# Performance work log

Measured on AMD Instinct MI355X. Metric: run time of the kernel, lower is better.

The kernel has to match this reference:

```python
import jax, jax.numpy as jnp
import numpy as np

EPS = 0.001  # ReEig clamp threshold (init epsilon)


def _eig_fn(x, fn):
    """Batched eigen-decomposition, apply fn to eigenvalues, reconstruct SPD."""
    w, v = jnp.linalg.eigh(x)              # w: [N,d], v: [N,d,d]
    return jnp.einsum('nik,nk,njk->nij', v, fn(w), v)


def reeig(x, eps=EPS):
    return _eig_fn(x, lambda w: jnp.maximum(w, eps))


def logeig(x):
    return _eig_fn(x, jnp.log)


def bimap(x, W):
    # W: [no, ni] (semi-orthogonal), out = W X W^T, SPD of size no
    return jnp.einsum('oi,nij,pj->nop', W, x, W)


def vech(x):
    # Half-vectorization of symmetric matrix; off-diagonal scaled by sqrt(2)
    d = x.shape[-1]
    iu = jnp.triu_indices(d)
    scale = jnp.where(iu[0] == iu[1], 1.0, jnp.sqrt(2.0)).astype(x.dtype)
    return x[:, iu[0], iu[1]] * scale


def _semi_orth(key, no, ni):
    a = jax.random.normal(key, (ni, ni), dtype=jnp.float32)
    q, _ = jnp.linalg.qr(a)
    return q[:no, :]  # [no, ni], rows orthonormal


def setup_inputs() -> dict:
    key = jax.random.key(0)
    kx, k1, k2, k3, kf, kb = jax.random.split(key, 6)
    N, D = 8192, 128
    A = jax.random.normal(kx, (N, D, D), dtype=jnp.float32)
    x = jnp.einsum('nij,nkj->nik', A, A) / D + 1e-3 * jnp.eye(D, dtype=jnp.float32)
    W1 = _semi_orth(k1, 64, 128)
    W2 = _semi_orth(k2, 32, 64)
    W3 = _semi_orth(k3, 16, 32)
    fdim = 16 * 17 // 2  # 136
    fc_w = jax.random.normal(kf, (4, fdim), dtype=jnp.float32) / jnp.sqrt(float(fdim))
    fc_b = jnp.zeros((4,), dtype=jnp.float32)
    return {"x": x, "W1": W1, "W2": W2, "W3": W3, "fc_w": fc_w, "fc_b": fc_b}


def reference(x, W1, W2, W3, fc_w, fc_b):
    h = reeig(bimap(x, W1))
    h = reeig(bimap(h, W2))
    h = reeig(bimap(h, W3))
    h = logeig(h)
    v = vech(h)                       # [N, 136] (dropout is identity in eval)
    return v @ fc_w.T + fc_b          # [N, 4]
```

## Files before the change

### kernel.cpp

```cpp
#include <hip/hip_runtime.h>
#include <math.h>
#include <stdint.h>


typedef __attribute__((ext_vector_type(4))) float f32x4;
typedef __attribute__((ext_vector_type(8))) short bf16x8;
typedef __attribute__((ext_vector_type(4))) unsigned int u32x4;

__constant__ float DCF[21] = {
    -0.98268864f,  1.26902401f, -0.40260548f,  0.17030534f, -0.08104560f,
     0.04113953f, -0.02175295f,  0.01183073f, -0.00656840f,  0.00370465f,
    -0.00211558f,  0.00122033f, -0.00070979f,  0.00041573f, -0.00024495f,
     0.00014506f, -0.00008629f,  0.00005153f, -0.00003088f,  0.00001856f,
    -0.00001119f};

struct Spl { unsigned int h01, h23, l01, l23; };

__device__ __forceinline__ unsigned cvtpk(float a, float b) {
  unsigned r;
  asm("v_cvt_pk_bf16_f32 %0, %1, %2" : "=v"(r) : "v"(a), "v"(b));
  return r;
}

__device__ __forceinline__ Spl split4(const float x[4]) {
  Spl s;
  s.h01 = cvtpk(x[0], x[1]);
  s.h23 = cvtpk(x[2], x[3]);
  const float h0 = __builtin_bit_cast(float, s.h01 << 16);
  const float h1 = __builtin_bit_cast(float, s.h01 & 0xffff0000u);
  const float h2 = __builtin_bit_cast(float, s.h23 << 16);
  const float h3 = __builtin_bit_cast(float, s.h23 & 0xffff0000u);
  s.l01 = cvtpk(x[0] - h0, x[1] - h1);
  s.l23 = cvtpk(x[2] - h2, x[3] - h3);
  return s;
}

__device__ __forceinline__ f32x4 mfma2(u32x4 ua, u32x4 ub, f32x4 acc) {
  return __builtin_amdgcn_mfma_f32_16x16x32_bf16(
      __builtin_bit_cast(bf16x8, ua), __builtin_bit_cast(bf16x8, ub), acc,
      0, 0, 0);
}

__device__ __forceinline__ f32x4 mmA(u32x4 ua, const Spl& b, f32x4 acc) {
  u32x4 ub1 = {b.h01, b.h23, b.h01, b.h23};
  u32x4 ub2 = {b.l01, b.l23, 0u, 0u};
  acc = mfma2(ua, ub1, acc);
  acc = mfma2(ua, ub2, acc);
  return acc;
}

__device__ __forceinline__ f32x4 mmAp(u32x4 ua, u32x4 bp, f32x4 acc) {
  u32x4 ub1 = {bp.x, bp.y, bp.x, bp.y};
  u32x4 ub2 = {bp.z, bp.w, 0u, 0u};
  acc = mfma2(ua, ub1, acc);
  acc = mfma2(ua, ub2, acc);
  return acc;
}

__device__ __forceinline__ f32x4 mmS(const Spl& a, const Spl& b) {
  u32x4 ua = {a.h01, a.h23, a.l01, a.l23};
  f32x4 z = {0.f, 0.f, 0.f, 0.f};
  return mmA(ua, b, z);
}

__global__ __launch_bounds__(256) void ka_weff(const float* __restrict__ W1,
                                               const float* __restrict__ W2,
                                               const float* __restrict__ W3,
                                               u32x4* __restrict__ WDg) {
  __shared__ float W21s[32 * 128];
  __shared__ float Ws[16 * 128];
  const int t = threadIdx.x;
  const int c = t & 127, rb = t >> 7;
  float acc[16];
#pragma unroll
  for (int rr = 0; rr < 16; ++rr) acc[rr] = 0.0f;
  for (int k = 0; k < 64; ++k) {
    const float w1 = W1[k * 128 + c];
#pragma unroll
    for (int rr = 0; rr < 16; ++rr)
      acc[rr] = fmaf(W2[(rb * 16 + rr) * 64 + k], w1, acc[rr]);
  }
#pragma unroll
  for (int rr = 0; rr < 16; ++rr) W21s[(rb * 16 + rr) * 128 + c] = acc[rr];
  __syncthreads();
  float a2[8];
#pragma unroll
  for (int rr = 0; rr < 8; ++rr) a2[rr] = 0.0f;
  for (int k = 0; k < 32; ++k) {
    const float w21 = W21s[k * 128 + c];
#pragma unroll
    for (int rr = 0; rr < 8; ++rr)
      a2[rr] = fmaf(W3[(rb * 8 + rr) * 32 + k], w21, a2[rr]);
  }
#pragma unroll
  for (int rr = 0; rr < 8; ++rr) Ws[(rb * 8 + rr) * 128 + c] = a2[rr];
  __syncthreads();
  {
    const int lane = t & 63, b0 = t >> 6;
    const int g = lane >> 4, cc = lane & 15;
#pragma unroll
    for (int p = 0; p < 2; ++p) {
      const int b = b0 + 4 * p;
      float x[4];
#pragma unroll
      for (int j = 0; j < 4; ++j) x[j] = Ws[cc * 128 + 16 * b + 4 * g + j];
      Spl s = split4(x);
      u32x4 v = {s.h01, s.h23, s.l01, s.l23};
      WDg[b * 64 + lane] = v;
    }
  }
}

#define NPERS 768

__global__ __launch_bounds__(256, 3) void kbc_fused(
    const float* __restrict__ X, const u32x4* __restrict__ WDg,
    const float* __restrict__ fcw, const float* __restrict__ fcb,
    float* __restrict__ out, int ngrp) {
  __shared__ __align__(16) u32x4 wdL[512];
  __shared__ __align__(16) float stg[4][2176];
  __shared__ float fcs[544];
  __shared__ float dcfL[21];
  __shared__ float fbb[4];

  const int t = threadIdx.x;
  wdL[t] = WDg[t];
  wdL[t + 256] = WDg[t + 256];
  for (int q = t; q < 544; q += 256) fcs[q] = fcw[q];
  if (t < 4) fbb[t] = fcb[t];
  if (t < 21) dcfL[t] = DCF[t];
  __syncthreads();

  const int w = t >> 6, l = t & 63;
  const int g = l >> 4, c = l & 15;
  const int r8 = l >> 3, s8 = l & 7;
  float* sg = stg[w];
  const f32x4 z4 = {0.f, 0.f, 0.f, 0.f};

#pragma unroll 1
  for (int grp = blockIdx.x; grp < ngrp; grp += NPERS) {
    const int n = grp * 4 + w;
    const float* xb = X + (size_t)n * 16384;

    f32x4 Aoff = z4, Adiag = z4, S0 = z4, S1 = z4;

#define LI_(RB) (2 * (((RB) + 2) >> 1))
#define LOADI(ARR, RB)                                                      \
  _Pragma("unroll")                                                         \
  for (int i = 0; i < LI_(RB); ++i)                                         \
    ARR[i] = __builtin_nontemporal_load(                                    \
        (const f32x4*)(xb + ((16 * (RB) + 8 * (i & 1) + r8) * 128 +         \
                             (i >> 1) * 32 + s8 * 4)));
#define STAGE(ARR, RB)                                                      \
  _Pragma("unroll")                                                         \
  for (int i = 0; i < LI_(RB); ++i)                                         \
    *(f32x4*)&sg[(8 * (i & 1) + r8) * 136 + (i >> 1) * 32 + s8 * 4] = ARR[i];

#define BODIES(RB)                                                          \
  {                                                                         \
    _Pragma("unroll")                                                       \
    for (int jb = 0; jb < (RB); ++jb) {                                     \
      f32x4 f = *(const f32x4*)&sg[c * 136 + jb * 16 + g * 4];              \
      float xx[4] = {f[0], f[1], f[2], f[3]};                               \
      Spl fx = split4(xx);                                                  \
      u32x4 ux = {fx.h01, fx.h23, fx.l01, fx.l23};                          \
      if (jb & 1) S1 = mmAp(ux, wdL[jb * 64 + l], S1);                      \
      else        S0 = mmAp(ux, wdL[jb * 64 + l], S0);                      \
    }                                                                       \
    {                                                                       \
      f32x4 f = *(const f32x4*)&sg[c * 136 + (RB) * 16 + g * 4];            \
      float xx[4] = {f[0], f[1], f[2], f[3]};                               \
      Spl fx = split4(xx);                                                  \
      u32x4 ux = {fx.h01, fx.h23, fx.l01, fx.l23};                          \
      const u32x4 wr = wdL[(RB) * 64 + l];                                  \
      f32x4 Sd = mmAp(ux, wr, z4);                                          \
      if ((RB) > 0) {                                                       \
        f32x4 St = S0 + S1;                                                 \
        float ss[4] = {St[0], St[1], St[2], St[3]};                         \
        Spl sS = split4(ss);                                                \
        Aoff = mmA(wr, sS, Aoff);                                           \
        S0 = z4; S1 = z4;                                                   \
      }                                                                     \
      float sd[4] = {Sd[0], Sd[1], Sd[2], Sd[3]};                           \
      Spl sD = split4(sd);                                                  \
      Adiag = mmA(wr, sD, Adiag);                                           \
    }                                                                       \
  }

    f32x4 rA[8], rB[8];
    LOADI(rA, 0)
    LOADI(rB, 1)
    STAGE(rA, 0)
    BODIES(0) LOADI(rA, 2) STAGE(rB, 1)
    BODIES(1) LOADI(rB, 3) STAGE(rA, 2)
    BODIES(2) LOADI(rA, 4) STAGE(rB, 3)
    BODIES(3) LOADI(rB, 5) STAGE(rA, 4)
    BODIES(4) LOADI(rA, 6) STAGE(rB, 5)
    BODIES(5) LOADI(rB, 7) STAGE(rA, 6)
    BODIES(6)              STAGE(rB, 7)
    BODIES(7)
#undef BODIES
#undef STAGE
#undef LOADI
#undef LI_

    f32x4 M;
    {
      const unsigned Ih01 = ((c == 4 * g + 0) ? 0x3F80u : 0u) |
                            ((c == 4 * g + 1) ? 0x3F800000u : 0u);
      const unsigned Ih23 = ((c == 4 * g + 2) ? 0x3F80u : 0u) |
                            ((c == 4 * g + 3) ? 0x3F800000u : 0u);
      const u32x4 uI = {Ih01, Ih23, Ih01, Ih23};
      float ao[4] = {Aoff[0], Aoff[1], Aoff[2], Aoff[3]};
      Spl sa = split4(ao);
      u32x4 uat = {sa.h01, sa.h23, sa.l01, sa.l23};
      M = mfma2(uat, uI, Aoff + Adiag);
    }

    float mac[4] = {M[0], M[1], M[2], M[3]};
    float dg[4];
#pragma unroll
    for (int j = 0; j < 4; ++j) dg[j] = (4 * g + j == c) ? 1.0f : 0.0f;

    float as[4];
#pragma unroll
    for (int j = 0; j < 4; ++j) as[j] = fabsf(mac[j]);
#pragma unroll
    for (int d = 1; d < 16; d <<= 1)
#pragma unroll
      for (int j = 0; j < 4; ++j) as[j] += __shfl_xor(as[j], d);
    float mx = fmaxf(fmaxf(as[0], as[1]), fmaxf(as[2], as[3]));
    mx = fmaxf(mx, __shfl_xor(mx, 16));
    mx = fmaxf(mx, __shfl_xor(mx, 32));
    const float s = mx, inv_s = 1.0f / mx;
    const float lnS = logf(s);

    const float k4b = 4.21052631f;
    const float k2b = 2.21052631f;

    float t2[4];
    const float sc1 = k4b * inv_s;
#pragma unroll
    for (int j = 0; j < 4; ++j) t2[j] = fmaf(mac[j], sc1, -k2b * dg[j]);
    const Spl sT2 = split4(t2);

    float u1[4], u2[4];
    {
      const float d20 = dcfL[20];
#pragma unroll
      for (int j = 0; j < 4; ++j) { u1[j] = d20 * dg[j]; u2[j] = 0.0f; }
    }
    Spl su1 = split4(u1);
#pragma unroll 1
    for (int k = 19; k >= 1; --k) {
      const float cf = dcfL[k];
      f32x4 p = mmS(sT2, su1);
      float un[4];
#pragma unroll
      for (int j = 0; j < 4; ++j) {
        un[j] = cf * dg[j] + p[j] - u2[j];
        u2[j] = u1[j];
        u1[j] = un[j];
      }
      su1 = split4(u1);
    }
    float U4[4];
    {
      f32x4 p = mmS(sT2, su1);
      const float d0 = dcfL[0] + lnS;
#pragma unroll
      for (int j = 0; j < 4; ++j) U4[j] = d0 * dg[j] + 0.5f * p[j] - u2[j];
    }

    float p4[4] = {0.0f, 0.0f, 0.0f, 0.0f};
#pragma unroll
    for (int j = 0; j < 4; ++j) {
      const int rw = 4 * g + j;
      const float scv = (rw == c) ? 1.0f : ((rw < c) ? 1.41421356237f : 0.0f);
      const float vv = scv * U4[j];
      const int idx = (rw * (31 - rw)) / 2 + c;
#pragma unroll
      for (int cc = 0; cc < 4; ++cc)
        p4[cc] = fmaf(fcs[cc * 136 + idx], vv, p4[cc]);
    }
#pragma unroll
    for (int d = 1; d < 64; d <<= 1)
#pragma unroll
      for (int cc = 0; cc < 4; ++cc) p4[cc] += __shfl_xor(p4[cc], d);
    if (l == 0) {
      float4 o;
      o.x = p4[0] + fbb[0]; o.y = p4[1] + fbb[1];
      o.z = p4[2] + fbb[2]; o.w = p4[3] + fbb[3];
      *(float4*)&out[(size_t)n * 4] = o;
    }
  }
}

extern "C" void kernel_launch(void* const* d_in, const int* in_sizes, int n_in,
                              void* d_out, int out_size, void* d_ws, size_t ws_size,
                              hipStream_t stream) {
  (void)n_in; (void)out_size; (void)ws_size;
  const float* x = (const float*)d_in[0];
  const float* W1 = (const float*)d_in[1];
  const float* W2 = (const float*)d_in[2];
  const float* W3 = (const float*)d_in[3];
  const float* fcw = (const float*)d_in[4];
  const float* fcb = (const float*)d_in[5];
  float* outp = (float*)d_out;

  const int N = in_sizes[0] / (128 * 128);
  u32x4* WDg = (u32x4*)d_ws;

  ka_weff<<<1, 256, 0, stream>>>(W1, W2, W3, WDg);
  kbc_fused<<<NPERS, 256, 0, stream>>>(x, WDg, fcw, fcb, outp, N / 4);
}
```

Measured before the change: 79.38 us.

## Prefetch next matrix's first row blocks across persistent-loop iterations

The persistent loop now gives each block a contiguous range of groups instead of a strided one. It issues the loads for the next matrix's first two row blocks during the tail of the current matrix, so the eigen/FC epilogue overlaps with memory latency. This raises register pressure because rA/rB stay live across the epilogue. The contiguous assignment also changes the access pattern across blocks.

```diff
diff --git a/kernel.cpp b/kernel.cpp
--- a/kernel.cpp
+++ b/kernel.cpp
@@ -137,19 +137,20 @@
   float* sg = stg[w];
   const f32x4 z4 = {0.f, 0.f, 0.f, 0.f};
 
-#pragma unroll 1
-  for (int grp = blockIdx.x; grp < ngrp; grp += NPERS) {
-    const int n = grp * 4 + w;
-    const float* xb = X + (size_t)n * 16384;
-
-    f32x4 Aoff = z4, Adiag = z4, S0 = z4, S1 = z4;
+  const int q_ = ngrp / NPERS, r_ = ngrp % NPERS;
+  const int bid = blockIdx.x;
+  const int start = bid * q_ + (bid < r_ ? bid : r_);
+  const int cnt = q_ + (bid < r_ ? 1 : 0);
+
+  int n = start * 4 + w;
+  const float* xb = X + (size_t)n * 16384;
 
 #define LI_(RB) (2 * (((RB) + 2) >> 1))
-#define LOADI(ARR, RB)                                                      \
+#define LOADI(ARR, BP, RB)                                                  \
   _Pragma("unroll")                                                         \
   for (int i = 0; i < LI_(RB); ++i)                                         \
     ARR[i] = __builtin_nontemporal_load(                                    \
-        (const f32x4*)(xb + ((16 * (RB) + 8 * (i & 1) + r8) * 128 +         \
+        (const f32x4*)(BP + ((16 * (RB) + 8 * (i & 1) + r8) * 128 +         \
                              (i >> 1) * 32 + s8 * 4)));
 #define STAGE(ARR, RB)                                                      \
   _Pragma("unroll")                                                         \
@@ -187,22 +188,28 @@
     }                                                                       \
   }
 
-    f32x4 rA[8], rB[8];
-    LOADI(rA, 0)
-    LOADI(rB, 1)
+  f32x4 rA[8], rB[8];
+  LOADI(rA, xb, 0)
+  LOADI(rB, xb, 1)
+
+#pragma unroll 1
+  for (int it = 0; it < cnt; ++it) {
+    const float* xn = xb + 4 * 16384;
+    const bool more = (it + 1 < cnt);
+
+    f32x4 Aoff = z4, Adiag = z4, S0 = z4, S1 = z4;
+
     STAGE(rA, 0)
-    BODIES(0) LOADI(rA, 2) STAGE(rB, 1)
-    BODIES(1) LOADI(rB, 3) STAGE(rA, 2)
-    BODIES(2) LOADI(rA, 4) STAGE(rB, 3)
-    BODIES(3) LOADI(rB, 5) STAGE(rA, 4)
-    BODIES(4) LOADI(rA, 6) STAGE(rB, 5)
-    BODIES(5) LOADI(rB, 7) STAGE(rA, 6)
-    BODIES(6)              STAGE(rB, 7)
+    BODIES(0) LOADI(rA, xb, 2) STAGE(rB, 1)
+    BODIES(1) LOADI(rB, xb, 3) STAGE(rA, 2)
+    BODIES(2) LOADI(rA, xb, 4) STAGE(rB, 3)
+    BODIES(3) LOADI(rB, xb, 5) STAGE(rA, 4)
+    BODIES(4) LOADI(rA, xb, 6) STAGE(rB, 5)
+    BODIES(5) LOADI(rB, xb, 7) STAGE(rA, 6)
+    if (more) { LOADI(rA, xn, 0) }
+    BODIES(6) STAGE(rB, 7)
+    if (more) { LOADI(rB, xn, 1) }
     BODIES(7)
-#undef BODIES
-#undef STAGE
-#undef LOADI
-#undef LI_
 
     f32x4 M;
     {
@@ -293,7 +300,14 @@
       o.z = p4[2] + fbb[2]; o.w = p4[3] + fbb[3];
       *(float4*)&out[(size_t)n * 4] = o;
     }
-  }
+
+    n += 4;
+    xb = xn;
+  }
+#undef BODIES
+#undef STAGE
+#undef LOADI
+#undef LI_
 }
 
 extern "C" void kernel_launch(void* const* d_in, const int* in_sizes, int n_in,
```

Result: faster. 77.82 us (-2.0%).
